# Performance work log

Hardware: AMD Instinct MI355X
Metric: run time of the kernel (lower is better)

Reference implementation:

```python
import jax, jax.numpy as jnp
import numpy as np

B, S, AS, E, H, V, P, HOPS = 256, 128, 5, 300, 300, 50000, 3, 3


def _lstm_dir(x, mask, w_ih, w_hh, b_ih, b_hh):
    # x: (B,S,E), mask: (B,S) bool. torch LSTM gate order: i,f,g,o.
    Bsz = x.shape[0]
    Hd = w_hh.shape[1]
    xT = jnp.swapaxes(x, 0, 1)                      # (S,B,E)
    mT = jnp.swapaxes(mask, 0, 1)[..., None]        # (S,B,1)

    def step(carry, inp):
        h, c = carry
        xt, mt = inp
        gates = xt @ w_ih.T + b_ih + h @ w_hh.T + b_hh
        i_g, f_g, g_g, o_g = jnp.split(gates, 4, axis=-1)
        c_new = jax.nn.sigmoid(f_g) * c + jax.nn.sigmoid(i_g) * jnp.tanh(g_g)
        h_new = jax.nn.sigmoid(o_g) * jnp.tanh(c_new)
        h2 = jnp.where(mt, h_new, h)
        c2 = jnp.where(mt, c_new, c)
        return (h2, c2), jnp.where(mt, h_new, 0.0)

    init = (jnp.zeros((Bsz, Hd), x.dtype), jnp.zeros((Bsz, Hd), x.dtype))
    _, out = jax.lax.scan(step, init, (xT, mT))
    return jnp.swapaxes(out, 0, 1)                  # (B,S,H), zero at pads


def _bilstm(x, lengths, params):
    (wif, whf, bif, bhf, wib, whb, bib, bhb) = params
    pos = jnp.arange(S)
    mask = pos[None, :] < lengths[:, None]          # (B,S)
    out_f = _lstm_dir(x, mask, wif, whf, bif, bhf)
    # per-sequence reversal for the backward direction
    rev_idx = jnp.clip(lengths[:, None] - 1 - pos[None, :], 0, S - 1)  # (B,S)
    x_rev = jnp.take_along_axis(x, rev_idx[..., None], axis=1)
    out_rev = _lstm_dir(x_rev, mask, wib, whb, bib, bhb)
    out_b = jnp.take_along_axis(out_rev, rev_idx[..., None], axis=1)
    out_b = jnp.where(mask[..., None], out_b, 0.0)
    return jnp.concatenate([out_f, out_b], axis=-1)  # (B,S,2H)


def _locationed_memory(memory, memory_len, left_len, aspect_len):
    idx = jnp.arange(S)[None, :]                    # (1,S)
    a_start = left_len[:, None]
    a_end = a_start + aspect_len[:, None]
    u = jnp.where(idx < a_start, idx - a_start,
                  jnp.where(idx < a_end, 0, idx - a_end + 1)).astype(memory.dtype)
    l = jnp.where(idx < a_start, a_start - idx,
                  jnp.where(idx < a_end, 0, idx - a_end + 1)).astype(memory.dtype)
    valid = idx < memory_len[:, None]
    u = jnp.where(valid, u, 0.0)
    w = jnp.where(valid, 1.0 - l / memory_len[:, None].astype(memory.dtype), 1.0)
    memory = memory * w[..., None]
    return jnp.concatenate([memory, u[..., None]], axis=-1)  # (B,S,2H+1)


def setup_inputs() -> dict:
    key = jax.random.key(0)
    ks = jax.random.split(key, 24)
    mem_len = jax.random.randint(ks[0], (B,), S // 2, S + 1)
    asp_len = jax.random.randint(ks[1], (B,), 1, AS + 1)
    left_len = jax.random.randint(ks[2], (B,), 0, 10000) % jnp.maximum(mem_len - asp_len, 1)
    pos_s = jnp.arange(S)[None, :]
    pos_a = jnp.arange(AS)[None, :]
    text_raw_indices = jnp.where(pos_s < mem_len[:, None],
                                 jax.random.randint(ks[3], (B, S), 1, V), 0)
    aspect_indices = jnp.where(pos_a < asp_len[:, None],
                               jax.random.randint(ks[4], (B, AS), 1, V), 0)
    text_left_indices = jnp.where(pos_s < left_len[:, None],
                                  jax.random.randint(ks[5], (B, S), 1, V), 0)

    def nrm(k, shape, scale=0.08):
        return (jax.random.normal(k, shape, dtype=jnp.float32) * scale)

    D = 2 * H + 1
    return {
        "text_raw_indices": text_raw_indices,
        "aspect_indices": aspect_indices,
        "text_left_indices": text_left_indices,
        "embedding": nrm(ks[6], (V, E), 0.3),
        "w_ih_f": nrm(ks[7], (4 * H, E)), "w_hh_f": nrm(ks[8], (4 * H, H)),
        "b_ih_f": nrm(ks[9], (4 * H,)), "b_hh_f": nrm(ks[10], (4 * H,)),
        "w_ih_b": nrm(ks[11], (4 * H, E)), "w_hh_b": nrm(ks[12], (4 * H, H)),
        "b_ih_b": nrm(ks[13], (4 * H,)), "b_hh_b": nrm(ks[14], (4 * H,)),
        "att_w": nrm(ks[15], (1, D + 2 * E)), "att_b": nrm(ks[16], (1,)),
        "gru_w_ih": nrm(ks[17], (3 * E, D)), "gru_w_hh": nrm(ks[18], (3 * E, E)),
        "gru_b_ih": nrm(ks[19], (3 * E,)), "gru_b_hh": nrm(ks[20], (3 * E,)),
        "dense_w": nrm(ks[21], (P, E)), "dense_b": nrm(ks[22], (P,)),
    }


def reference(text_raw_indices, aspect_indices, text_left_indices, embedding,
              w_ih_f, w_hh_f, b_ih_f, b_hh_f, w_ih_b, w_hh_b, b_ih_b, b_hh_b,
              att_w, att_b, gru_w_ih, gru_w_hh, gru_b_ih, gru_b_hh,
              dense_w, dense_b):
    left_len = jnp.sum(text_left_indices != 0, axis=-1)
    memory_len = jnp.sum(text_raw_indices != 0, axis=-1)
    aspect_len = jnp.sum(aspect_indices != 0, axis=-1)

    memory = embedding[text_raw_indices]                          # (B,S,E)
    memory = _bilstm(memory, memory_len,
                     (w_ih_f, w_hh_f, b_ih_f, b_hh_f, w_ih_b, w_hh_b, b_ih_b, b_hh_b))
    memory = _locationed_memory(memory, memory_len, left_len, aspect_len)  # (B,S,2H+1)

    aspect = embedding[aspect_indices].sum(axis=1) / aspect_len[:, None].astype(jnp.float32)
    et = jnp.zeros_like(aspect)                                   # (B,E)

    for _ in range(HOPS):
        et_b = jnp.broadcast_to(et[:, None, :], (B, S, E))
        asp_b = jnp.broadcast_to(aspect[:, None, :], (B, S, E))
        feat = jnp.concatenate([memory, et_b, asp_b], axis=-1)    # (B,S,2H+1+2E)
        g = feat @ att_w.T + att_b                                # (B,S,1)
        alpha = jax.nn.softmax(g, axis=1)
        i_t = jnp.einsum('bs,bsd->bd', alpha[..., 0], memory)     # (B,2H+1)
        # torch GRUCell: gate order r,z,n
        gi = i_t @ gru_w_ih.T + gru_b_ih
        gh = et @ gru_w_hh.T + gru_b_hh
        gi_r, gi_z, gi_n = jnp.split(gi, 3, axis=-1)
        gh_r, gh_z, gh_n = jnp.split(gh, 3, axis=-1)
        r = jax.nn.sigmoid(gi_r + gh_r)
        z = jax.nn.sigmoid(gi_z + gh_z)
        n = jnp.tanh(gi_n + r * gh_n)
        et = (1.0 - z) * n + z * et

    return et @ dense_w.T + dense_b                               # (B,P)
```

## Files before the change

kernel.cpp:

```cpp
#include <hip/hip_runtime.h>
#include <hip/hip_bf16.h>
#include <math.h>

#define BB 256
#define SS 128
#define EE 300
#define HH 300
#define G4 1200
#define DD 601
#define DP 608
#define ASZ 5
#define PP 3

typedef __attribute__((ext_vector_type(8))) short bf16x8s;
typedef __attribute__((ext_vector_type(4))) float f32x4;

union V16 { uint4 q; bf16x8s v; ushort u[8]; };

static __device__ __forceinline__ float sigf(float x){ return 1.0f/(1.0f+expf(-x)); }
static __device__ __forceinline__ float bf2f(ushort u){ unsigned int x = ((unsigned int)u)<<16; return __uint_as_float(x); }
static __device__ __forceinline__ ushort f2bf(float f){ __hip_bfloat16 h = __float2bfloat16(f); return *reinterpret_cast<ushort*>(&h); }

__global__ void lengths_kernel(const int* __restrict__ traw, const int* __restrict__ tleft,
                               const int* __restrict__ aidx, int* __restrict__ lens){
  int b = blockIdx.x, tid = threadIdx.x;
  __shared__ int cnt[3];
  if(tid<3) cnt[tid]=0;
  __syncthreads();
  if(traw[b*SS+tid]!=0)  atomicAdd(&cnt[0],1);
  if(tleft[b*SS+tid]!=0) atomicAdd(&cnt[1],1);
  if(tid<ASZ && aidx[b*ASZ+tid]!=0) atomicAdd(&cnt[2],1);
  __syncthreads();
  if(tid==0){ lens[b]=cnt[0]; lens[BB+b]=cnt[1]; lens[2*BB+b]=cnt[2]; }
}

__global__ void wprep_kernel(const float* __restrict__ whhf, const float* __restrict__ whhb,
                             __hip_bfloat16* __restrict__ Wn){
  int np = blockIdx.x;
  int dir = blockIdx.y;
  int k = threadIdx.x;
  const float* src = dir ? whhb : whhf;
  int hl = np>>2, g = np&3;
  float v = (hl<300 && k<300) ? src[(size_t)(g*300+hl)*300 + k] : 0.0f;
  Wn[((size_t)dir*1280 + np)*320 + k] = __float2bfloat16(v);
}

__global__ __launch_bounds__(512)
void xproj_mfma(const int* __restrict__ idxrows, const float* __restrict__ emb,
                const float* __restrict__ w_ih, const float* __restrict__ b_ih,
                const float* __restrict__ b_hh, __hip_bfloat16* __restrict__ Xp){
  __shared__ uint4 As16[128*8];
  __shared__ uint4 Bs16[128*8];
  __shared__ int rowidx[128];
  int m0 = blockIdx.y*128;
  int n0 = blockIdx.x*128;
  int tid = threadIdx.x;
  int w = tid>>6, l = tid&63;
  int col = l&15, kgrp = l>>4;
  int wm = w>>1, wn = w&1;
  if(tid<128) rowidx[tid] = idxrows[m0+tid];
  f32x4 acc[2][4];
#pragma unroll
  for(int a=0;a<2;a++)
#pragma unroll
    for(int bq=0;bq<4;bq++){ acc[a][bq].x=0.f; acc[a][bq].y=0.f; acc[a][bq].z=0.f; acc[a][bq].w=0.f; }
  __syncthreads();
  for(int c=0;c<5;c++){
    int k0 = c*64;
    if(c>0) __syncthreads();
#pragma unroll
    for(int j=0;j<2;j++){
      int s = tid*2 + j;
      int row = s>>3, q = s&7;
      int kb = k0 + q*8;
      const float* ar = emb + (size_t)rowidx[row]*EE;
      V16 pk;
      if(kb+7 < 300){
        float4 f0 = *(const float4*)(ar+kb);
        float4 f1 = *(const float4*)(ar+kb+4);
        pk.u[0]=f2bf(f0.x); pk.u[1]=f2bf(f0.y); pk.u[2]=f2bf(f0.z); pk.u[3]=f2bf(f0.w);
        pk.u[4]=f2bf(f1.x); pk.u[5]=f2bf(f1.y); pk.u[6]=f2bf(f1.z); pk.u[7]=f2bf(f1.w);
      } else {
#pragma unroll
        for(int e=0;e<8;e++){ float v = (kb+e<300) ? ar[kb+e] : 0.0f; pk.u[e]=f2bf(v); }
      }
      As16[row*8 + (q^(row&7))] = pk.q;
      int np = n0 + row;
      V16 pb;
      if(np < G4){
        const float* br = w_ih + (size_t)((np&3)*300 + (np>>2))*EE;
        if(kb+7 < 300){
          float4 f0 = *(const float4*)(br+kb);
          float4 f1 = *(const float4*)(br+kb+4);
          pb.u[0]=f2bf(f0.x); pb.u[1]=f2bf(f0.y); pb.u[2]=f2bf(f0.z); pb.u[3]=f2bf(f0.w);
          pb.u[4]=f2bf(f1.x); pb.u[5]=f2bf(f1.y); pb.u[6]=f2bf(f1.z); pb.u[7]=f2bf(f1.w);
        } else {
#pragma unroll
          for(int e=0;e<8;e++){ float v = (kb+e<300) ? br[kb+e] : 0.0f; pb.u[e]=f2bf(v); }
        }
      } else {
        pb.q = make_uint4(0,0,0,0);
      }
      Bs16[row*8 + (q^(row&7))] = pb.q;
    }
    __syncthreads();
#pragma unroll
    for(int kc=0;kc<2;kc++){
      int q = kc*4 + kgrp;
      V16 ua0, ua1, ub0, ub1, ub2, ub3;
      int ra0 = wm*32 + col, ra1 = wm*32 + 16 + col;
      ua0.q = As16[ra0*8 + (q^(ra0&7))];
      ua1.q = As16[ra1*8 + (q^(ra1&7))];
      int rb0 = wn*64 + col;
      ub0.q = Bs16[rb0*8 + (q^(rb0&7))];
      ub1.q = Bs16[(rb0+16)*8 + (q^((rb0+16)&7))];
      ub2.q = Bs16[(rb0+32)*8 + (q^((rb0+32)&7))];
      ub3.q = Bs16[(rb0+48)*8 + (q^((rb0+48)&7))];
      acc[0][0] = __builtin_amdgcn_mfma_f32_16x16x32_bf16(ua0.v, ub0.v, acc[0][0], 0,0,0);
      acc[1][0] = __builtin_amdgcn_mfma_f32_16x16x32_bf16(ua1.v, ub0.v, acc[1][0], 0,0,0);
      acc[0][1] = __builtin_amdgcn_mfma_f32_16x16x32_bf16(ua0.v, ub1.v, acc[0][1], 0,0,0);
      acc[1][1] = __builtin_amdgcn_mfma_f32_16x16x32_bf16(ua1.v, ub1.v, acc[1][1], 0,0,0);
      acc[0][2] = __builtin_amdgcn_mfma_f32_16x16x32_bf16(ua0.v, ub2.v, acc[0][2], 0,0,0);
      acc[1][2] = __builtin_amdgcn_mfma_f32_16x16x32_bf16(ua1.v, ub2.v, acc[1][2], 0,0,0);
      acc[0][3] = __builtin_amdgcn_mfma_f32_16x16x32_bf16(ua0.v, ub3.v, acc[0][3], 0,0,0);
      acc[1][3] = __builtin_amdgcn_mfma_f32_16x16x32_bf16(ua1.v, ub3.v, acc[1][3], 0,0,0);
    }
  }
#pragma unroll
  for(int in=0;in<4;in++){
    int np = n0 + wn*64 + in*16 + col;
    if(np >= G4) continue;
    int orig = (np&3)*300 + (np>>2);
    float bias = b_ih[orig] + b_hh[orig];
#pragma unroll
    for(int im=0;im<2;im++){
#pragma unroll
      for(int r=0;r<4;r++){
        int m = m0 + wm*32 + im*16 + kgrp*4 + r;
        float v = acc[im][in][r] + bias;
        Xp[(size_t)m*G4 + np] = __float2bfloat16(v);
      }
    }
  }
}

__global__ __launch_bounds__(512,2)
void lstm_self(const __hip_bfloat16* __restrict__ Xp, const __hip_bfloat16* __restrict__ Wn,
               float* __restrict__ mem, const int* __restrict__ lens){
  __shared__ uint4 hA4[640];
  __shared__ float gbuf[16][1296];
  __shared__ float c_s[16][304];
  int bid = blockIdx.x;
  int dir = bid>>4, mbt = bid&15;
  int b0 = mbt*16;
  int tid = threadIdx.x;
  int w = tid>>6, l = tid&63;
  int col = l&15, kgrp = l>>4, colx7 = col&7;
  int pm = tid>>5;
  int pl = tid&31;
  int Lm = lens[b0+pm];

  for(int i=tid;i<640;i+=512) hA4[i] = make_uint4(0,0,0,0);
  for(int i=tid;i<16*304;i+=512) ((float*)c_s)[i] = 0.0f;

  int tMax = 0;
  for(int m=0;m<16;m++){ int L = lens[b0+m]; tMax = L>tMax ? L : tMax; }

  const __hip_bfloat16* Xpd = Xp + (size_t)dir*BB*SS*G4;
  const uint4* wp = reinterpret_cast<const uint4*>(Wn + ((size_t)dir*1280 + w*160)*320);
  __syncthreads();

  for(int t=0;t<tMax;++t){
    bool act = (t < Lm);
    int sx = dir ? (Lm-1-t) : t;
    uint2 xpr[10];
    if(act){
      const uint2* xs = reinterpret_cast<const uint2*>(Xpd + ((size_t)(b0+pm)*SS + sx)*G4) + pl;
#pragma unroll
      for(int j=0;j<10;j++){ if(pl + 32*j < 300) xpr[j] = xs[32*j]; }
    }
    __syncthreads();
    f32x4 acc[10];
#pragma unroll
    for(int i=0;i<10;i++){ acc[i].x=0.f; acc[i].y=0.f; acc[i].z=0.f; acc[i].w=0.f; }
#pragma unroll
    for(int kc=0;kc<10;kc++){
      V16 ua; ua.q = hA4[col*40 + ((kc*4+kgrp) ^ colx7)];
#pragma unroll
      for(int i=0;i<10;i++){
        V16 ub; ub.q = wp[(i*16+col)*40 + kc*4 + kgrp];
        acc[i] = __builtin_amdgcn_mfma_f32_16x16x32_bf16(ua.v, ub.v, acc[i], 0,0,0);
      }
    }
#pragma unroll
    for(int i=0;i<10;i++){
      int np = w*160 + i*16 + col;
#pragma unroll
      for(int r=0;r<4;r++) gbuf[kgrp*4+r][np] = acc[i][r];
    }
    __syncthreads();
    if(act){
#pragma unroll
      for(int j=0;j<10;j++){
        int hl = pl + 32*j;
        if(hl >= 300) continue;
        f32x4 g4 = *reinterpret_cast<const f32x4*>(&gbuf[pm][hl*4]);
        union{ uint2 u2; ushort s[4]; } xv; xv.u2 = xpr[j];
        float ig = sigf(g4.x + bf2f(xv.s[0]));
        float fg = sigf(g4.y + bf2f(xv.s[1]));
        float gg = tanhf(g4.z + bf2f(xv.s[2]));
        float og = sigf(g4.w + bf2f(xv.s[3]));
        float cn = fg*c_s[pm][hl] + ig*gg;
        float hn = og*tanhf(cn);
        c_s[pm][hl] = cn;
        mem[((size_t)(b0+pm)*SS + sx)*DP + dir*HH + hl] = hn;
        int q = hl>>3, e = hl&7;
        reinterpret_cast<ushort*>(&hA4[pm*40 + (q ^ (pm&7))])[e] = f2bf(hn);
      }
    }
  }
}

__global__ void loc_score_kernel(float* __restrict__ mem, const float* __restrict__ att_w,
                                 const int* __restrict__ lens, float* __restrict__ score){
  int bs = blockIdx.x;
  int b = bs/SS, s = bs%SS;
  int tid = threadIdx.x;
  int len = lens[b], left = lens[BB+b], alen = lens[2*BB+b];
  int a_start = left, a_end = left + alen;
  float uf = (s<a_start) ? (float)(s-a_start) : (s<a_end ? 0.f : (float)(s-a_end+1));
  float lf = (s<a_start) ? (float)(a_start-s) : (s<a_end ? 0.f : (float)(s-a_end+1));
  float w  = 1.f - lf/(float)len;
  float u  = (s<len) ? uf : 0.f;
  float partial = 0.f;
  float* row = mem + (size_t)bs*DP;
  if(s < len){
    for(int e=tid;e<600;e+=128){
      float v = row[e]*w;
      row[e] = v;
      partial += v*att_w[e];
    }
  }
  if(tid==0){
    row[600] = u;
    partial += u*att_w[600];
  }
  __shared__ float red[128];
  red[tid]=partial; __syncthreads();
  for(int s2=64;s2>0;s2>>=1){ if(tid<s2) red[tid]+=red[tid+s2]; __syncthreads(); }
  if(tid==0) score[bs]=red[0];
}

__global__ void softmax_it_kernel(const float* __restrict__ score, const float* __restrict__ mem,
                                  float* __restrict__ i_t){
  int b = blockIdx.x, tid = threadIdx.x;
  __shared__ float sc[SS];
  __shared__ float red[SS];
  float v = score[b*SS+tid];
  red[tid]=v; __syncthreads();
  for(int s2=64;s2>0;s2>>=1){ if(tid<s2) red[tid]=fmaxf(red[tid],red[tid+s2]); __syncthreads(); }
  float m = red[0]; __syncthreads();
  float e = expf(v-m);
  sc[tid]=e; red[tid]=e; __syncthreads();
  for(int s2=64;s2>0;s2>>=1){ if(tid<s2) red[tid]+=red[tid+s2]; __syncthreads(); }
  float inv = 1.f/red[0]; __syncthreads();
  sc[tid] *= inv;
  __syncthreads();
  float acc[5]={0.f,0.f,0.f,0.f,0.f};
  for(int s=0;s<SS;s++){
    float a = sc[s];
    const float* row = mem + ((size_t)b*SS+s)*DP;
#pragma unroll
    for(int q=0;q<5;q++){
      int d = q*128+tid;
      if(d<DD) acc[q] += a*row[d];
    }
  }
#pragma unroll
  for(int q=0;q<5;q++){
    int d = q*128+tid;
    if(d<DD) i_t[(size_t)b*DP+d] = acc[q];
  }
}

__global__ __launch_bounds__(320)
void gi_kernel(const float* __restrict__ i_t, const float* __restrict__ gwih,
               const float* __restrict__ gbih, float* __restrict__ gi){
  int b = blockIdx.x, tid = threadIdx.x;
  __shared__ float it[DD];
  for(int d=tid;d<DD;d+=320) it[d]=i_t[(size_t)b*DP+d];
  __syncthreads();
  for(int n=tid;n<900;n+=320){
    const float* wr = gwih + (size_t)n*DD;
    float s=0.f;
    for(int d=0;d<DD;d++) s += wr[d]*it[d];
    gi[(size_t)b*900+n] = s + gbih[n];
  }
}

__global__ __launch_bounds__(320)
void hops_kernel(const float* __restrict__ gi, const float* __restrict__ gwhh,
                 const float* __restrict__ gbhh, const float* __restrict__ dw,
                 const float* __restrict__ db, float* __restrict__ out){
  int b = blockIdx.x, tid = threadIdx.x;
  __shared__ float et_s[HH];
  float gir=0.f,giz=0.f,gin=0.f,bhr=0.f,bhz=0.f,bhn=0.f;
  if(tid<300){
    et_s[tid]=0.f;
    gir = gi[(size_t)b*900+tid];
    giz = gi[(size_t)b*900+300+tid];
    gin = gi[(size_t)b*900+600+tid];
    bhr = gbhh[tid]; bhz = gbhh[300+tid]; bhn = gbhh[600+tid];
  }
  __syncthreads();
  for(int hop=0;hop<3;hop++){
    float etn=0.f;
    if(tid<300){
      const float* wr = gwhh + (size_t)tid*HH;
      const float* wz = gwhh + (size_t)(300+tid)*HH;
      const float* wn = gwhh + (size_t)(600+tid)*HH;
      float ghr=bhr, ghz=bhz, ghn=bhn;
      for(int d=0;d<HH;d++){
        float e = et_s[d];
        ghr += wr[d]*e; ghz += wz[d]*e; ghn += wn[d]*e;
      }
      float r = sigf(gir+ghr);
      float z = sigf(giz+ghz);
      float n = tanhf(gin + r*ghn);
      etn = (1.f-z)*n + z*et_s[tid];
    }
    __syncthreads();
    if(tid<300) et_s[tid]=etn;
    __syncthreads();
  }
  if(tid<192){
    int p = tid/64, lane = tid%64;
    float partial = 0.f;
    for(int e=lane;e<HH;e+=64) partial += et_s[e]*dw[(size_t)p*HH+e];
    for(int off=32;off>0;off>>=1) partial += __shfl_down(partial, off);
    if(lane==0) out[(size_t)b*PP+p] = partial + db[p];
  }
}

extern "C" void kernel_launch(void* const* d_in, const int* in_sizes, int n_in,
                              void* d_out, int out_size, void* d_ws, size_t ws_size,
                              hipStream_t stream){
  (void)in_sizes; (void)n_in; (void)out_size; (void)ws_size;
  const int*   traw  = (const int*)  d_in[0];
  const int*   aidx  = (const int*)  d_in[1];
  const int*   tleft = (const int*)  d_in[2];
  const float* emb   = (const float*)d_in[3];
  const float* wihf  = (const float*)d_in[4];
  const float* whhf  = (const float*)d_in[5];
  const float* bihf  = (const float*)d_in[6];
  const float* bhhf  = (const float*)d_in[7];
  const float* wihb  = (const float*)d_in[8];
  const float* whhb  = (const float*)d_in[9];
  const float* bihb  = (const float*)d_in[10];
  const float* bhhb  = (const float*)d_in[11];
  const float* attw  = (const float*)d_in[12];
  const float* gwih  = (const float*)d_in[14];
  const float* gwhh  = (const float*)d_in[15];
  const float* gbih  = (const float*)d_in[16];
  const float* gbhh  = (const float*)d_in[17];
  const float* dw    = (const float*)d_in[18];
  const float* db    = (const float*)d_in[19];
  float* out = (float*)d_out;

  char* ws = (char*)d_ws;
  size_t off = 0;
  auto alloc = [&](size_t bytes)->void*{
    void* p = ws + off;
    off += (bytes + 255) & ~(size_t)255;
    return p;
  };
  __hip_bfloat16* Xp  = (__hip_bfloat16*)alloc((size_t)2*BB*SS*G4*2);
  float* mem   = (float*)alloc((size_t)BB*SS*DP*4);
  __hip_bfloat16* Wn  = (__hip_bfloat16*)alloc((size_t)2*1280*320*2);
  int*   lens  = (int*)  alloc(3*BB*sizeof(int));
  float* score = (float*)alloc((size_t)BB*SS*4);
  float* i_t   = (float*)alloc((size_t)BB*DP*4);
  float* gi    = (float*)alloc((size_t)BB*900*4);

  hipMemsetAsync(mem, 0, (size_t)BB*SS*DP*4, stream);

  lengths_kernel<<<BB,128,0,stream>>>(traw, tleft, aidx, lens);
  wprep_kernel<<<dim3(1280,2),320,0,stream>>>(whhf, whhb, Wn);

  xproj_mfma<<<dim3(10,256),512,0,stream>>>(traw, emb, wihf, bihf, bhhf, Xp);
  xproj_mfma<<<dim3(10,256),512,0,stream>>>(traw, emb, wihb, bihb, bhhb, Xp + (size_t)BB*SS*G4);

  lstm_self<<<32,512,0,stream>>>(Xp, Wn, mem, lens);

  loc_score_kernel<<<BB*SS,128,0,stream>>>(mem, attw, lens, score);
  softmax_it_kernel<<<BB,128,0,stream>>>(score, mem, i_t);
  gi_kernel<<<BB,320,0,stream>>>(i_t, gwih, gbih, gi);
  hops_kernel<<<BB,320,0,stream>>>(gi, gwhh, gbhh, dw, db, out);
}
```

Before: 3.549 ms.

## Restructure LSTM recurrence with register cell state, LDS weights and prepacked input weights

The recurrent LSTM kernel moves from 512 to 1024 threads. Each wave computes a transposed MFMA tile whose output lanes map directly to (batch, hidden) gate quadruples, so the gbuf shared-memory round trip and one barrier per step go away. Cell state stays in registers, the hidden state is double-buffered, and part of W_hh is cached in LDS while the other waves software-prefetch their weights from global memory. Separately, W_ih and the biases are prepacked to bf16 once, both directions' input projections run in a single launch, and sigmoid uses the fast __expf, which slightly reduces accuracy.

```diff
diff --git a/kernel.cpp b/kernel.cpp
--- a/kernel.cpp
+++ b/kernel.cpp
@@ -17,7 +17,7 @@
 
 union V16 { uint4 q; bf16x8s v; ushort u[8]; };
 
-static __device__ __forceinline__ float sigf(float x){ return 1.0f/(1.0f+expf(-x)); }
+static __device__ __forceinline__ float sigf(float x){ return 1.0f/(1.0f+__expf(-x)); }
 static __device__ __forceinline__ float bf2f(ushort u){ unsigned int x = ((unsigned int)u)<<16; return __uint_as_float(x); }
 static __device__ __forceinline__ ushort f2bf(float f){ __hip_bfloat16 h = __float2bfloat16(f); return *reinterpret_cast<ushort*>(&h); }
 
@@ -45,15 +45,37 @@
   Wn[((size_t)dir*1280 + np)*320 + k] = __float2bfloat16(v);
 }
 
+__global__ void wihprep_kernel(const float* __restrict__ wihf, const float* __restrict__ wihb,
+                               const float* __restrict__ bihf, const float* __restrict__ bhhf,
+                               const float* __restrict__ bihb, const float* __restrict__ bhhb,
+                               __hip_bfloat16* __restrict__ Wihn, float* __restrict__ biasn){
+  int np = blockIdx.x;
+  int dir = blockIdx.y;
+  int k = threadIdx.x;
+  const float* src = dir ? wihb : wihf;
+  int hl = np>>2, g = np&3;
+  int orig = g*300 + hl;
+  float v = (hl<300 && k<300) ? src[(size_t)orig*EE + k] : 0.0f;
+  Wihn[((size_t)dir*1280 + np)*320 + k] = __float2bfloat16(v);
+  if(k==0){
+    float bsum = 0.0f;
+    if(hl<300) bsum = (dir ? (bihb[orig]+bhhb[orig]) : (bihf[orig]+bhhf[orig]));
+    biasn[(size_t)dir*1280 + np] = bsum;
+  }
+}
+
 __global__ __launch_bounds__(512)
 void xproj_mfma(const int* __restrict__ idxrows, const float* __restrict__ emb,
-                const float* __restrict__ w_ih, const float* __restrict__ b_ih,
-                const float* __restrict__ b_hh, __hip_bfloat16* __restrict__ Xp){
+                const __hip_bfloat16* __restrict__ Wihn, const float* __restrict__ biasn,
+                __hip_bfloat16* __restrict__ Xp){
   __shared__ uint4 As16[128*8];
   __shared__ uint4 Bs16[128*8];
   __shared__ int rowidx[128];
+  int dir = blockIdx.z;
   int m0 = blockIdx.y*128;
   int n0 = blockIdx.x*128;
+  const uint4* wihn4 = reinterpret_cast<const uint4*>(Wihn) + (size_t)dir*1280*40;
+  __hip_bfloat16* Xpd = Xp + (size_t)dir*BB*SS*G4;
   int tid = threadIdx.x;
   int w = tid>>6, l = tid&63;
   int col = l&15, kgrp = l>>4;
@@ -66,14 +88,11 @@
     for(int bq=0;bq<4;bq++){ acc[a][bq].x=0.f; acc[a][bq].y=0.f; acc[a][bq].z=0.f; acc[a][bq].w=0.f; }
   __syncthreads();
   for(int c=0;c<5;c++){
-    int k0 = c*64;
     if(c>0) __syncthreads();
-#pragma unroll
-    for(int j=0;j<2;j++){
-      int s = tid*2 + j;
-      int row = s>>3, q = s&7;
-      int kb = k0 + q*8;
-      const float* ar = emb + (size_t)rowidx[row]*EE;
+    for(int i=tid;i<1024;i+=512){
+      int r = i>>3, q = i&7;
+      int kb = c*64 + q*8;
+      const float* ar = emb + (size_t)rowidx[r]*EE;
       V16 pk;
       if(kb+7 < 300){
         float4 f0 = *(const float4*)(ar+kb);
@@ -84,24 +103,8 @@
 #pragma unroll
         for(int e=0;e<8;e++){ float v = (kb+e<300) ? ar[kb+e] : 0.0f; pk.u[e]=f2bf(v); }
       }
-      As16[row*8 + (q^(row&7))] = pk.q;
-      int np = n0 + row;
-      V16 pb;
-      if(np < G4){
-        const float* br = w_ih + (size_t)((np&3)*300 + (np>>2))*EE;
-        if(kb+7 < 300){
-          float4 f0 = *(const float4*)(br+kb);
-          float4 f1 = *(const float4*)(br+kb+4);
-          pb.u[0]=f2bf(f0.x); pb.u[1]=f2bf(f0.y); pb.u[2]=f2bf(f0.z); pb.u[3]=f2bf(f0.w);
-          pb.u[4]=f2bf(f1.x); pb.u[5]=f2bf(f1.y); pb.u[6]=f2bf(f1.z); pb.u[7]=f2bf(f1.w);
-        } else {
-#pragma unroll
-          for(int e=0;e<8;e++){ float v = (kb+e<300) ? br[kb+e] : 0.0f; pb.u[e]=f2bf(v); }
-        }
-      } else {
-        pb.q = make_uint4(0,0,0,0);
-      }
-      Bs16[row*8 + (q^(row&7))] = pb.q;
+      As16[r*8 + (q^(r&7))] = pk.q;
+      Bs16[r*8 + (q^(r&7))] = wihn4[(size_t)(n0+r)*40 + c*8 + q];
     }
     __syncthreads();
 #pragma unroll
@@ -130,94 +133,116 @@
   for(int in=0;in<4;in++){
     int np = n0 + wn*64 + in*16 + col;
     if(np >= G4) continue;
-    int orig = (np&3)*300 + (np>>2);
-    float bias = b_ih[orig] + b_hh[orig];
+    float bias = biasn[(size_t)dir*1280 + np];
 #pragma unroll
     for(int im=0;im<2;im++){
 #pragma unroll
       for(int r=0;r<4;r++){
         int m = m0 + wm*32 + im*16 + kgrp*4 + r;
         float v = acc[im][in][r] + bias;
-        Xp[(size_t)m*G4 + np] = __float2bfloat16(v);
-      }
-    }
-  }
-}
-
-__global__ __launch_bounds__(512,2)
+        Xpd[(size_t)m*G4 + np] = __float2bfloat16(v);
+      }
+    }
+  }
+}
+
+__global__ __launch_bounds__(1024)
 void lstm_self(const __hip_bfloat16* __restrict__ Xp, const __hip_bfloat16* __restrict__ Wn,
                float* __restrict__ mem, const int* __restrict__ lens){
-  __shared__ uint4 hA4[640];
-  __shared__ float gbuf[16][1296];
-  __shared__ float c_s[16][304];
+  __shared__ uint4 Wlds[160*40];
+  __shared__ uint4 hbuf[2][640];
   int bid = blockIdx.x;
   int dir = bid>>4, mbt = bid&15;
   int b0 = mbt*16;
   int tid = threadIdx.x;
   int w = tid>>6, l = tid&63;
-  int col = l&15, kgrp = l>>4, colx7 = col&7;
-  int pm = tid>>5;
-  int pl = tid&31;
-  int Lm = lens[b0+pm];
-
-  for(int i=tid;i<640;i+=512) hA4[i] = make_uint4(0,0,0,0);
-  for(int i=tid;i<16*304;i+=512) ((float*)c_s)[i] = 0.0f;
-
+  int col = l&15, kgrp = l>>4;
+  int colx7 = col&7;
+
+  const __hip_bfloat16* Xpd = Xp + (size_t)dir*BB*SS*G4;
+  const uint4* wpD = reinterpret_cast<const uint4*>(Wn + (size_t)dir*1280*320);
+  const uint4* wp  = wpD + (size_t)w*80*40;
+
+  for(int i=tid;i<1280;i+=1024) ((uint4*)hbuf)[i] = make_uint4(0,0,0,0);
+  for(int i=tid;i<6400;i+=1024){
+    int r = i/40, q = i - r*40;
+    Wlds[r*40 + (q ^ (r&7))] = wpD[i];
+  }
+
+  int Lm = lens[b0+col];
   int tMax = 0;
   for(int m=0;m<16;m++){ int L = lens[b0+m]; tMax = L>tMax ? L : tMax; }
 
-  const __hip_bfloat16* Xpd = Xp + (size_t)dir*BB*SS*G4;
-  const uint4* wp = reinterpret_cast<const uint4*>(Wn + ((size_t)dir*1280 + w*160)*320);
+  float c_r[5] = {0.f,0.f,0.f,0.f,0.f};
   __syncthreads();
 
   for(int t=0;t<tMax;++t){
+    int cur = t&1, nxt = cur^1;
     bool act = (t < Lm);
     int sx = dir ? (Lm-1-t) : t;
-    uint2 xpr[10];
+    uint2 xpr[5];
     if(act){
-      const uint2* xs = reinterpret_cast<const uint2*>(Xpd + ((size_t)(b0+pm)*SS + sx)*G4) + pl;
-#pragma unroll
-      for(int j=0;j<10;j++){ if(pl + 32*j < 300) xpr[j] = xs[32*j]; }
+      const uint2* xb = reinterpret_cast<const uint2*>(Xpd + ((size_t)(b0+col)*SS + sx)*G4);
+#pragma unroll
+      for(int i=0;i<5;i++){
+        int hl = w*20 + i*4 + kgrp;
+        if(hl < 300) xpr[i] = xb[hl];
+      }
+    }
+    f32x4 acc[5];
+#pragma unroll
+    for(int i=0;i<5;i++){ acc[i].x=0.f; acc[i].y=0.f; acc[i].z=0.f; acc[i].w=0.f; }
+    if(w < 2){
+#pragma unroll 2
+      for(int kc=0;kc<10;kc++){
+        V16 ua; ua.q = hbuf[cur][col*40 + ((kc*4+kgrp) ^ colx7)];
+#pragma unroll
+        for(int i=0;i<5;i++){
+          int r = w*80 + i*16 + col;
+          V16 wv; wv.q = Wlds[r*40 + ((kc*4+kgrp) ^ (r&7))];
+          acc[i] = __builtin_amdgcn_mfma_f32_16x16x32_bf16(wv.v, ua.v, acc[i], 0,0,0);
+        }
+      }
+    } else if(w < 15){
+      V16 wr2[2][5];
+#pragma unroll
+      for(int i=0;i<5;i++) wr2[0][i].q = wp[(i*16+col)*40 + kgrp];
+#pragma unroll
+      for(int kc=0;kc<10;kc++){
+        int pb = kc&1;
+        if(kc<9){
+#pragma unroll
+          for(int i=0;i<5;i++) wr2[pb^1][i].q = wp[(i*16+col)*40 + (kc+1)*4 + kgrp];
+        }
+        V16 ua; ua.q = hbuf[cur][col*40 + ((kc*4+kgrp) ^ colx7)];
+#pragma unroll
+        for(int i=0;i<5;i++)
+          acc[i] = __builtin_amdgcn_mfma_f32_16x16x32_bf16(wr2[pb][i].v, ua.v, acc[i], 0,0,0);
+      }
+    }
+#pragma unroll
+    for(int i=0;i<5;i++){
+      int hl = w*20 + i*4 + kgrp;
+      if(hl >= 300) continue;
+      int q = hl>>3, e = hl&7;
+      ushort hbits;
+      if(act){
+        union{ uint2 u; ushort s[4]; } xv; xv.u = xpr[i];
+        float ig = sigf(acc[i][0] + bf2f(xv.s[0]));
+        float fg = sigf(acc[i][1] + bf2f(xv.s[1]));
+        float gg = tanhf(acc[i][2] + bf2f(xv.s[2]));
+        float og = sigf(acc[i][3] + bf2f(xv.s[3]));
+        float cn = fg*c_r[i] + ig*gg;
+        float hn = og*tanhf(cn);
+        c_r[i] = cn;
+        mem[((size_t)(b0+col)*SS + sx)*DP + dir*HH + hl] = hn;
+        hbits = f2bf(hn);
+      } else {
+        hbits = reinterpret_cast<const ushort*>(&hbuf[cur][col*40 + (q ^ colx7)])[e];
+      }
+      reinterpret_cast<ushort*>(&hbuf[nxt][col*40 + (q ^ colx7)])[e] = hbits;
     }
     __syncthreads();
-    f32x4 acc[10];
-#pragma unroll
-    for(int i=0;i<10;i++){ acc[i].x=0.f; acc[i].y=0.f; acc[i].z=0.f; acc[i].w=0.f; }
-#pragma unroll
-    for(int kc=0;kc<10;kc++){
-      V16 ua; ua.q = hA4[col*40 + ((kc*4+kgrp) ^ colx7)];
-#pragma unroll
-      for(int i=0;i<10;i++){
-        V16 ub; ub.q = wp[(i*16+col)*40 + kc*4 + kgrp];
-        acc[i] = __builtin_amdgcn_mfma_f32_16x16x32_bf16(ua.v, ub.v, acc[i], 0,0,0);
-      }
-    }
-#pragma unroll
-    for(int i=0;i<10;i++){
-      int np = w*160 + i*16 + col;
-#pragma unroll
-      for(int r=0;r<4;r++) gbuf[kgrp*4+r][np] = acc[i][r];
-    }
-    __syncthreads();
-    if(act){
-#pragma unroll
-      for(int j=0;j<10;j++){
-        int hl = pl + 32*j;
-        if(hl >= 300) continue;
-        f32x4 g4 = *reinterpret_cast<const f32x4*>(&gbuf[pm][hl*4]);
-        union{ uint2 u2; ushort s[4]; } xv; xv.u2 = xpr[j];
-        float ig = sigf(g4.x + bf2f(xv.s[0]));
-        float fg = sigf(g4.y + bf2f(xv.s[1]));
-        float gg = tanhf(g4.z + bf2f(xv.s[2]));
-        float og = sigf(g4.w + bf2f(xv.s[3]));
-        float cn = fg*c_s[pm][hl] + ig*gg;
-        float hn = og*tanhf(cn);
-        c_s[pm][hl] = cn;
-        mem[((size_t)(b0+pm)*SS + sx)*DP + dir*HH + hl] = hn;
-        int q = hl>>3, e = hl&7;
-        reinterpret_cast<ushort*>(&hA4[pm*40 + (q ^ (pm&7))])[e] = f2bf(hn);
-      }
-    }
   }
 }
 
@@ -374,9 +399,11 @@
     off += (bytes + 255) & ~(size_t)255;
     return p;
   };
-  __hip_bfloat16* Xp  = (__hip_bfloat16*)alloc((size_t)2*BB*SS*G4*2);
+  __hip_bfloat16* Xp   = (__hip_bfloat16*)alloc((size_t)2*BB*SS*G4*2);
   float* mem   = (float*)alloc((size_t)BB*SS*DP*4);
-  __hip_bfloat16* Wn  = (__hip_bfloat16*)alloc((size_t)2*1280*320*2);
+  __hip_bfloat16* Wn   = (__hip_bfloat16*)alloc((size_t)2*1280*320*2);
+  __hip_bfloat16* Wihn = (__hip_bfloat16*)alloc((size_t)2*1280*320*2);
+  float* biasn = (float*)alloc((size_t)2*1280*4);
   int*   lens  = (int*)  alloc(3*BB*sizeof(int));
   float* score = (float*)alloc((size_t)BB*SS*4);
   float* i_t   = (float*)alloc((size_t)BB*DP*4);
@@ -386,11 +413,11 @@
 
   lengths_kernel<<<BB,128,0,stream>>>(traw, tleft, aidx, lens);
   wprep_kernel<<<dim3(1280,2),320,0,stream>>>(whhf, whhb, Wn);
-
-  xproj_mfma<<<dim3(10,256),512,0,stream>>>(traw, emb, wihf, bihf, bhhf, Xp);
-  xproj_mfma<<<dim3(10,256),512,0,stream>>>(traw, emb, wihb, bihb, bhhb, Xp + (size_t)BB*SS*G4);
-
-  lstm_self<<<32,512,0,stream>>>(Xp, Wn, mem, lens);
+  wihprep_kernel<<<dim3(1280,2),320,0,stream>>>(wihf, wihb, bihf, bhhf, bihb, bhhb, Wihn, biasn);
+
+  xproj_mfma<<<dim3(10,256,2),512,0,stream>>>(traw, emb, Wihn, biasn, Xp);
+
+  lstm_self<<<32,1024,0,stream>>>(Xp, Wn, mem, lens);
 
   loc_score_kernel<<<BB*SS,128,0,stream>>>(mem, attw, lens, score);
   softmax_it_kernel<<<BB,128,0,stream>>>(score, mem, i_t);
```

Measured after the change: 3.692 ms. 4.0% more time.
